# Performance work log

Hardware: AMD Instinct MI355X
Metric: run time of the kernel (lower is better)

## Reference

```python
import jax, jax.numpy as jnp
import numpy as np

N_USERS = 200000
N_ITEMS = 200000
N = N_USERS + N_ITEMS
D = 64
NNZ = 12800000
N_LAYERS = 3


def setup_inputs() -> dict:
    key = jax.random.key(0)
    ks = jax.random.split(key, 9)
    adj_rows = jax.random.randint(ks[0], (NNZ,), 0, N, dtype=jnp.int32)
    adj_cols = jax.random.randint(ks[1], (NNZ,), 0, N, dtype=jnp.int32)
    # positive normalized-ish edge weights, like D^-1/2 A D^-1/2 entries
    adj_vals = jax.random.uniform(ks[2], (NNZ,), dtype=jnp.float32) * 0.05
    user_emb = jax.random.normal(ks[3], (N_USERS, D), dtype=jnp.float32) * 0.1
    item_emb = jax.random.normal(ks[4], (N_ITEMS, D), dtype=jnp.float32) * 0.1
    w_scale = 1.0 / np.sqrt(D)
    gc_w = jax.random.normal(ks[5], (N_LAYERS, D, D), dtype=jnp.float32) * w_scale
    gc_b = jax.random.normal(ks[6], (N_LAYERS, D), dtype=jnp.float32) * 0.01
    bi_w = jax.random.normal(ks[7], (N_LAYERS, D, D), dtype=jnp.float32) * w_scale
    bi_b = jax.random.normal(ks[8], (N_LAYERS, D), dtype=jnp.float32) * 0.01
    return {"adj_rows": adj_rows, "adj_cols": adj_cols, "adj_vals": adj_vals,
            "user_emb": user_emb, "item_emb": item_emb,
            "gc_w": gc_w, "gc_b": gc_b, "bi_w": bi_w, "bi_b": bi_b}


def _spmm(rows, cols, vals, x):
    # COO sparse [N,N] @ dense [N,D] -> gather source rows, scale, scatter-add
    gathered = x[cols] * vals[:, None]          # [nnz, D]
    return jax.ops.segment_sum(gathered, rows, num_segments=N)  # [N, D]


def reference(adj_rows, adj_cols, adj_vals, user_emb, item_emb,
              gc_w, gc_b, bi_w, bi_b):
    ego = jnp.concatenate([user_emb, item_emb], axis=0)          # [N, D]
    all_emb = [ego]
    for i in range(N_LAYERS):
        side = _spmm(adj_rows, adj_cols, adj_vals, ego)          # [N, D]
        sum_e = jax.nn.leaky_relu(side @ gc_w[i].T + gc_b[i])    # GC branch
        bi_e = jax.nn.leaky_relu((ego * side) @ bi_w[i].T + bi_b[i])  # Bi branch
        ego = sum_e + bi_e                                       # dropout p=0 -> identity
        nrm = jnp.maximum(jnp.linalg.norm(ego, axis=1, keepdims=True), 1e-12)
        all_emb.append(ego / nrm)                                # F.normalize(p=2, dim=1)
    all_e = jnp.concatenate(all_emb, axis=1)                     # [N, D*(L+1)]
    return all_e[:N_USERS], all_e[N_USERS:]
```

## Files before the change

kernel.cpp:

```cpp
#include <hip/hip_runtime.h>
#include <stdint.h>

#define N_USERS 200000
#define N_ITEMS 200000
#define NTOT    400000
#define DD      64
#define NNZ     12800000

typedef unsigned short u16;
typedef float f4 __attribute__((ext_vector_type(4)));
typedef short s8 __attribute__((ext_vector_type(8)));

__device__ __forceinline__ float bf2f(u16 u){
  union { unsigned int i; float f; } x; x.i = ((unsigned int)u) << 16; return x.f;
}
__device__ __forceinline__ u16 f2bf(float f){
  unsigned int i = __float_as_uint(f);
  unsigned int r = (i + 0x7FFFu + ((i >> 16) & 1u)) >> 16;
  return (u16)r;
}

__global__ __launch_bounds__(256) void k_init(const float* __restrict__ ue,
                                              const float* __restrict__ ie,
                                              u16* __restrict__ ego,
                                              float* __restrict__ out){
  int t = blockIdx.x * 256 + threadIdx.x;
  float v = (t < N_USERS * DD) ? ue[t] : ie[t - N_USERS * DD];
  ego[t] = f2bf(v);
  int row = t >> 6, col = t & 63;
  out[row * 256 + col] = v;
}

__global__ __launch_bounds__(256) void k_hist(const int* __restrict__ rows,
                                              int* __restrict__ cnt){
  int e = blockIdx.x * 256 + threadIdx.x;
  atomicAdd(&cnt[rows[e]], 1);
}

__global__ __launch_bounds__(256) void k_scan1(const int* __restrict__ cnt,
                                               int* __restrict__ off,
                                               int* __restrict__ bsum){
  __shared__ int s[256];
  int i = blockIdx.x * 256 + threadIdx.x;
  int v = (i < NTOT) ? cnt[i] : 0;
  s[threadIdx.x] = v;
  __syncthreads();
  #pragma unroll
  for (int d = 1; d < 256; d <<= 1){
    int t = (threadIdx.x >= d) ? s[threadIdx.x - d] : 0;
    __syncthreads();
    s[threadIdx.x] += t;
    __syncthreads();
  }
  int incl = s[threadIdx.x];
  if (i < NTOT) off[i] = incl - v;
  if (threadIdx.x == 255) bsum[blockIdx.x] = incl;
}

__global__ __launch_bounds__(256) void k_scan2(int* __restrict__ bsum, int nb){
  __shared__ int s[256];
  __shared__ int carry_s;
  if (threadIdx.x == 0) carry_s = 0;
  __syncthreads();
  for (int base = 0; base < nb; base += 256){
    int i = base + threadIdx.x;
    int v = (i < nb) ? bsum[i] : 0;
    s[threadIdx.x] = v;
    __syncthreads();
    #pragma unroll
    for (int d = 1; d < 256; d <<= 1){
      int t = (threadIdx.x >= d) ? s[threadIdx.x - d] : 0;
      __syncthreads();
      s[threadIdx.x] += t;
      __syncthreads();
    }
    int incl = s[threadIdx.x];
    int c = carry_s;
    __syncthreads();
    if (i < nb) bsum[i] = c + incl - v;
    if (threadIdx.x == 255) carry_s = c + incl;
    __syncthreads();
  }
}

__global__ __launch_bounds__(256) void k_scan3(int* __restrict__ off,
                                               const int* __restrict__ bsum,
                                               int* __restrict__ cursor){
  int i = blockIdx.x * 256 + threadIdx.x;
  if (i < NTOT){
    int o = off[i] + bsum[i >> 8];
    off[i] = o;
    cursor[i] = o;
  }
  if (i == 0) off[NTOT] = NNZ;
}

__global__ __launch_bounds__(256) void k_scatter(const int* __restrict__ rows,
                                                 const int* __restrict__ cols,
                                                 const float* __restrict__ vals,
                                                 int* __restrict__ cursor,
                                                 uint2* __restrict__ edges){
  int e = blockIdx.x * 256 + threadIdx.x;
  int r = rows[e];
  int pos = atomicAdd(&cursor[r], 1);
  edges[pos] = make_uint2((unsigned)cols[e], __float_as_uint(vals[e]));
}

__global__ __launch_bounds__(256) void k_spmm(const int* __restrict__ off,
                                              const uint2* __restrict__ edges,
                                              const u16* __restrict__ ego,
                                              u16* __restrict__ side){
  int wid  = (blockIdx.x * 256 + threadIdx.x) >> 6;
  int lane = threadIdx.x & 63;
  int s0 = off[wid], s1 = off[wid + 1];
  float acc = 0.0f;
  int e = s0;
  for (; e + 1 < s1; e += 2){
    uint2 e0 = edges[e];
    uint2 e1 = edges[e + 1];
    float x0 = bf2f(ego[(unsigned)e0.x * 64u + lane]);
    float x1 = bf2f(ego[(unsigned)e1.x * 64u + lane]);
    acc += __uint_as_float(e0.y) * x0;
    acc += __uint_as_float(e1.y) * x1;
  }
  if (e < s1){
    uint2 e0 = edges[e];
    acc += __uint_as_float(e0.y) * bf2f(ego[(unsigned)e0.x * 64u + lane]);
  }
  side[wid * 64 + lane] = f2bf(acc);
}

__global__ __launch_bounds__(256) void k_fused(const u16* __restrict__ side,
                                               const u16* __restrict__ ego_in,
                                               u16* __restrict__ ego_out,
                                               float* __restrict__ out,
                                               const float* __restrict__ gw,
                                               const float* __restrict__ gb,
                                               const float* __restrict__ bw,
                                               const float* __restrict__ bb,
                                               int layer){
  int lane = threadIdx.x & 63;
  int wave = threadIdx.x >> 6;
  int rowbase = blockIdx.x * 64 + wave * 16;
  int m = lane & 15, quad = lane >> 4;

  const float* gwL = gw + layer * 4096;
  const float* bwL = bw + layer * 4096;

  union F8 { s8 v; u16 h[8]; };

  F8 as0, as1, ae0, ae1, ap0, ap1;
  int arow = (rowbase + m) * 64 + quad * 8;
  as0.v = *(const s8*)(side + arow);
  as1.v = *(const s8*)(side + arow + 32);
  ae0.v = *(const s8*)(ego_in + arow);
  ae1.v = *(const s8*)(ego_in + arow + 32);
  #pragma unroll
  for (int j = 0; j < 8; j++){
    ap0.h[j] = f2bf(bf2f(ae0.h[j]) * bf2f(as0.h[j]));
    ap1.h[j] = f2bf(bf2f(ae1.h[j]) * bf2f(as1.h[j]));
  }

  F8 bg[4][2], bww[4][2];
  #pragma unroll
  for (int t = 0; t < 4; t++){
    #pragma unroll
    for (int kb = 0; kb < 2; kb++){
      int widx = (t * 16 + m) * 64 + kb * 32 + quad * 8;
      #pragma unroll
      for (int j = 0; j < 8; j++){
        bg[t][kb].h[j]  = f2bf(gwL[widx + j]);
        bww[t][kb].h[j] = f2bf(bwL[widx + j]);
      }
    }
  }

  f4 ag[4], ab[4];
  #pragma unroll
  for (int t = 0; t < 4; t++){
    ag[t] = (f4){0.f, 0.f, 0.f, 0.f};
    ab[t] = (f4){0.f, 0.f, 0.f, 0.f};
  }

  #pragma unroll
  for (int t = 0; t < 4; t++){
    ag[t] = __builtin_amdgcn_mfma_f32_16x16x32_bf16(as0.v, bg[t][0].v, ag[t], 0, 0, 0);
    ag[t] = __builtin_amdgcn_mfma_f32_16x16x32_bf16(as1.v, bg[t][1].v, ag[t], 0, 0, 0);
    ab[t] = __builtin_amdgcn_mfma_f32_16x16x32_bf16(ap0.v, bww[t][0].v, ab[t], 0, 0, 0);
    ab[t] = __builtin_amdgcn_mfma_f32_16x16x32_bf16(ap1.v, bww[t][1].v, ab[t], 0, 0, 0);
  }

  float ev[4][4];
  #pragma unroll
  for (int t = 0; t < 4; t++){
    float gcb = gb[layer * 64 + t * 16 + m];
    float bib = bb[layer * 64 + t * 16 + m];
    #pragma unroll
    for (int r = 0; r < 4; r++){
      float x = ag[t][r] + gcb; x = (x > 0.f) ? x : 0.01f * x;
      float y = ab[t][r] + bib; y = (y > 0.f) ? y : 0.01f * y;
      ev[t][r] = x + y;
    }
  }

  float inv[4];
  #pragma unroll
  for (int r = 0; r < 4; r++){
    float p = 0.f;
    #pragma unroll
    for (int t = 0; t < 4; t++) p += ev[t][r] * ev[t][r];
    p += __shfl_xor(p, 1);
    p += __shfl_xor(p, 2);
    p += __shfl_xor(p, 4);
    p += __shfl_xor(p, 8);
    inv[r] = 1.0f / fmaxf(sqrtf(p), 1e-12f);
  }

  #pragma unroll
  for (int t = 0; t < 4; t++){
    #pragma unroll
    for (int r = 0; r < 4; r++){
      int row = rowbase + quad * 4 + r;
      int col = t * 16 + m;
      ego_out[row * 64 + col] = f2bf(ev[t][r]);
      out[row * 256 + (layer + 1) * 64 + col] = ev[t][r] * inv[r];
    }
  }
}

extern "C" void kernel_launch(void* const* d_in, const int* in_sizes, int n_in,
                              void* d_out, int out_size, void* d_ws, size_t ws_size,
                              hipStream_t stream) {
  const int*   rows = (const int*)d_in[0];
  const int*   cols = (const int*)d_in[1];
  const float* vals = (const float*)d_in[2];
  const float* ue   = (const float*)d_in[3];
  const float* ie   = (const float*)d_in[4];
  const float* gw   = (const float*)d_in[5];
  const float* gb   = (const float*)d_in[6];
  const float* bw   = (const float*)d_in[7];
  const float* bb   = (const float*)d_in[8];
  float* out = (float*)d_out;

  char* ws = (char*)d_ws;
  u16*   ego    = (u16*)(ws + 0);
  u16*   side   = (u16*)(ws + 51200000);
  uint2* edges  = (uint2*)(ws + 102400000);
  int*   cnt    = (int*)(ws + 204800000);
  int*   off    = (int*)(ws + 206400000);
  int*   cursor = (int*)(ws + 208000256);
  int*   bsum   = (int*)(ws + 209600256);

  hipMemsetAsync(cnt, 0, NTOT * sizeof(int), stream);

  k_init<<<(NTOT * DD) / 256, 256, 0, stream>>>(ue, ie, ego, out);
  k_hist<<<NNZ / 256, 256, 0, stream>>>(rows, cnt);
  k_scan1<<<(NTOT + 255) / 256, 256, 0, stream>>>(cnt, off, bsum);
  k_scan2<<<1, 256, 0, stream>>>(bsum, (NTOT + 255) / 256);
  k_scan3<<<(NTOT + 255) / 256, 256, 0, stream>>>(off, bsum, cursor);
  k_scatter<<<NNZ / 256, 256, 0, stream>>>(rows, cols, vals, cursor, edges);

  for (int l = 0; l < 3; l++){
    k_spmm<<<(NTOT * 64) / 256, 256, 0, stream>>>(off, edges, ego, side);
    k_fused<<<NTOT / 64, 256, 0, stream>>>(side, ego, ego, out,
                                           gw, gb, bw, bb, l);
  }
}
```

Measured before the change: 4.150 ms.

## Replace global-atomic COO-to-CSR build with two-pass bucketed partition sort

Replaces the per-edge global histogram, three-kernel scan and per-edge global-atomic scatter with a two-level radix partition. Edges are first bucketed by row>>10 using shared-memory histograms into a temp buffer that aliases the ego workspace. Each bucket is then locally sorted by the low row bits in shared memory, which also writes the row offsets. This targets global atomic contention and random scatter writes, at the cost of an extra pass over the edges and packing the column and local row into one 32-bit key.

```diff
diff --git a/kernel.cpp b/kernel.cpp
--- a/kernel.cpp
+++ b/kernel.cpp
@@ -6,6 +6,7 @@
 #define NTOT    400000
 #define DD      64
 #define NNZ     12800000
+#define NB      391
 
 typedef unsigned short u16;
 typedef float f4 __attribute__((ext_vector_type(4)));
@@ -31,79 +32,115 @@
   out[row * 256 + col] = v;
 }
 
-__global__ __launch_bounds__(256) void k_hist(const int* __restrict__ rows,
-                                              int* __restrict__ cnt){
-  int e = blockIdx.x * 256 + threadIdx.x;
-  atomicAdd(&cnt[rows[e]], 1);
-}
-
-__global__ __launch_bounds__(256) void k_scan1(const int* __restrict__ cnt,
-                                               int* __restrict__ off,
-                                               int* __restrict__ bsum){
-  __shared__ int s[256];
-  int i = blockIdx.x * 256 + threadIdx.x;
-  int v = (i < NTOT) ? cnt[i] : 0;
-  s[threadIdx.x] = v;
+__global__ __launch_bounds__(256) void k_chist(const int* __restrict__ rows,
+                                               int* __restrict__ cnt_b){
+  __shared__ int h[NB];
+  for (int i = threadIdx.x; i < NB; i += 256) h[i] = 0;
+  __syncthreads();
+  for (int e = blockIdx.x * 256 + threadIdx.x; e < NNZ; e += gridDim.x * 256)
+    atomicAdd(&h[rows[e] >> 10], 1);
+  __syncthreads();
+  for (int i = threadIdx.x; i < NB; i += 256)
+    if (h[i]) atomicAdd(&cnt_b[i], h[i]);
+}
+
+__global__ __launch_bounds__(512) void k_cscan(const int* __restrict__ cnt_b,
+                                               int* __restrict__ cstart,
+                                               int* __restrict__ ccursor,
+                                               int* __restrict__ off){
+  __shared__ int s[512];
+  int t = threadIdx.x;
+  int v = (t < NB) ? cnt_b[t] : 0;
+  s[t] = v;
+  __syncthreads();
+  #pragma unroll
+  for (int d = 1; d < 512; d <<= 1){
+    int u = (t >= d) ? s[t - d] : 0;
+    __syncthreads();
+    s[t] += u;
+    __syncthreads();
+  }
+  int excl = s[t] - v;
+  if (t < NB){ cstart[t] = excl; ccursor[t] = excl; }
+  if (t == NB - 1) cstart[NB] = excl + v;
+  if (t == 0) off[NTOT] = NNZ;
+}
+
+__global__ __launch_bounds__(512) void k_part(const int* __restrict__ rows,
+                                              const int* __restrict__ cols,
+                                              const float* __restrict__ vals,
+                                              int* __restrict__ ccursor,
+                                              uint2* __restrict__ tmp){
+  __shared__ int h[512];
+  int tid = threadIdx.x;
+  int base = blockIdx.x * 4096;
+  h[tid] = 0;
+  __syncthreads();
+  int myb[8]; int myrank[8]; unsigned mykey[8], myval[8];
+  #pragma unroll
+  for (int k = 0; k < 8; k++){
+    int e = base + k * 512 + tid;
+    int r = rows[e];
+    unsigned c = (unsigned)cols[e];
+    float v = vals[e];
+    int b = r >> 10;
+    myb[k] = b;
+    mykey[k] = ((unsigned)(r & 1023) << 19) | c;
+    myval[k] = __float_as_uint(v);
+    myrank[k] = atomicAdd(&h[b], 1);
+  }
+  __syncthreads();
+  int cnt = h[tid];
+  int gb = 0;
+  if (tid < NB && cnt > 0) gb = atomicAdd(&ccursor[tid], cnt);
+  __syncthreads();
+  h[tid] = gb;
+  __syncthreads();
+  #pragma unroll
+  for (int k = 0; k < 8; k++)
+    tmp[h[myb[k]] + myrank[k]] = make_uint2(mykey[k], myval[k]);
+}
+
+__global__ __launch_bounds__(256) void k_fine(const int* __restrict__ cstart,
+                                              const uint2* __restrict__ tmp,
+                                              int* __restrict__ off,
+                                              uint2* __restrict__ edges){
+  __shared__ int rh[1024];
+  __shared__ int sc[256];
+  int b = blockIdx.x, tid = threadIdx.x;
+  int s = cstart[b], e = cstart[b + 1];
+  for (int i = tid; i < 1024; i += 256) rh[i] = 0;
+  __syncthreads();
+  for (int i = s + tid; i < e; i += 256)
+    atomicAdd(&rh[tmp[i].x >> 19], 1);
+  __syncthreads();
+  int base4 = tid * 4;
+  int a0 = rh[base4], a1 = rh[base4 + 1], a2 = rh[base4 + 2], a3 = rh[base4 + 3];
+  int tsum = a0 + a1 + a2 + a3;
+  sc[tid] = tsum;
   __syncthreads();
   #pragma unroll
   for (int d = 1; d < 256; d <<= 1){
-    int t = (threadIdx.x >= d) ? s[threadIdx.x - d] : 0;
+    int u = (tid >= d) ? sc[tid - d] : 0;
     __syncthreads();
-    s[threadIdx.x] += t;
+    sc[tid] += u;
     __syncthreads();
   }
-  int incl = s[threadIdx.x];
-  if (i < NTOT) off[i] = incl - v;
-  if (threadIdx.x == 255) bsum[blockIdx.x] = incl;
-}
-
-__global__ __launch_bounds__(256) void k_scan2(int* __restrict__ bsum, int nb){
-  __shared__ int s[256];
-  __shared__ int carry_s;
-  if (threadIdx.x == 0) carry_s = 0;
-  __syncthreads();
-  for (int base = 0; base < nb; base += 256){
-    int i = base + threadIdx.x;
-    int v = (i < nb) ? bsum[i] : 0;
-    s[threadIdx.x] = v;
-    __syncthreads();
-    #pragma unroll
-    for (int d = 1; d < 256; d <<= 1){
-      int t = (threadIdx.x >= d) ? s[threadIdx.x - d] : 0;
-      __syncthreads();
-      s[threadIdx.x] += t;
-      __syncthreads();
-    }
-    int incl = s[threadIdx.x];
-    int c = carry_s;
-    __syncthreads();
-    if (i < nb) bsum[i] = c + incl - v;
-    if (threadIdx.x == 255) carry_s = c + incl;
-    __syncthreads();
-  }
-}
-
-__global__ __launch_bounds__(256) void k_scan3(int* __restrict__ off,
-                                               const int* __restrict__ bsum,
-                                               int* __restrict__ cursor){
-  int i = blockIdx.x * 256 + threadIdx.x;
-  if (i < NTOT){
-    int o = off[i] + bsum[i >> 8];
-    off[i] = o;
-    cursor[i] = o;
-  }
-  if (i == 0) off[NTOT] = NNZ;
-}
-
-__global__ __launch_bounds__(256) void k_scatter(const int* __restrict__ rows,
-                                                 const int* __restrict__ cols,
-                                                 const float* __restrict__ vals,
-                                                 int* __restrict__ cursor,
-                                                 uint2* __restrict__ edges){
-  int e = blockIdx.x * 256 + threadIdx.x;
-  int r = rows[e];
-  int pos = atomicAdd(&cursor[r], 1);
-  edges[pos] = make_uint2((unsigned)cols[e], __float_as_uint(vals[e]));
+  int excl = sc[tid] - tsum;
+  int r0 = excl, r1 = excl + a0, r2 = excl + a0 + a1, r3 = excl + a0 + a1 + a2;
+  rh[base4] = r0; rh[base4 + 1] = r1; rh[base4 + 2] = r2; rh[base4 + 3] = r3;
+  int rows_in = min(1024, NTOT - b * 1024);
+  if (base4     < rows_in) off[b * 1024 + base4]     = s + r0;
+  if (base4 + 1 < rows_in) off[b * 1024 + base4 + 1] = s + r1;
+  if (base4 + 2 < rows_in) off[b * 1024 + base4 + 2] = s + r2;
+  if (base4 + 3 < rows_in) off[b * 1024 + base4 + 3] = s + r3;
+  __syncthreads();
+  for (int i = s + tid; i < e; i += 256){
+    uint2 ed = tmp[i];
+    unsigned k = ed.x >> 19;
+    int pos = atomicAdd(&rh[k], 1);
+    edges[s + pos] = make_uint2(ed.x & 0x7FFFFu, ed.y);
+  }
 }
 
 __global__ __launch_bounds__(256) void k_spmm(const int* __restrict__ off,
@@ -246,19 +283,20 @@
   u16*   ego    = (u16*)(ws + 0);
   u16*   side   = (u16*)(ws + 51200000);
   uint2* edges  = (uint2*)(ws + 102400000);
-  int*   cnt    = (int*)(ws + 204800000);
-  int*   off    = (int*)(ws + 206400000);
-  int*   cursor = (int*)(ws + 208000256);
-  int*   bsum   = (int*)(ws + 209600256);
-
-  hipMemsetAsync(cnt, 0, NTOT * sizeof(int), stream);
+  uint2* tmp    = (uint2*)(ws + 0);
+  int*   off    = (int*)(ws + 204800000);
+  int*   cstart = (int*)(ws + 206400032);
+  int*   ccursor= (int*)(ws + 206401632);
+  int*   cnt_b  = (int*)(ws + 206403232);
+
+  hipMemsetAsync(cnt_b, 0, NB * sizeof(int), stream);
+
+  k_chist<<<1024, 256, 0, stream>>>(rows, cnt_b);
+  k_cscan<<<1, 512, 0, stream>>>(cnt_b, cstart, ccursor, off);
+  k_part<<<NNZ / 4096, 512, 0, stream>>>(rows, cols, vals, ccursor, tmp);
+  k_fine<<<NB, 256, 0, stream>>>(cstart, tmp, off, edges);
 
   k_init<<<(NTOT * DD) / 256, 256, 0, stream>>>(ue, ie, ego, out);
-  k_hist<<<NNZ / 256, 256, 0, stream>>>(rows, cnt);
-  k_scan1<<<(NTOT + 255) / 256, 256, 0, stream>>>(cnt, off, bsum);
-  k_scan2<<<1, 256, 0, stream>>>(bsum, (NTOT + 255) / 256);
-  k_scan3<<<(NTOT + 255) / 256, 256, 0, stream>>>(off, bsum, cursor);
-  k_scatter<<<NNZ / 256, 256, 0, stream>>>(rows, cols, vals, cursor, edges);
 
   for (int l = 0; l < 3; l++){
     k_spmm<<<(NTOT * 64) / 256, 256, 0, stream>>>(off, edges, ego, side);
```

After: 3.364 ms. 18.9% less time.
